# Performance work log

Hardware: AMD Instinct MI355X
Metric: run time of the kernel (lower is better)

## Reference

```python
import jax, jax.numpy as jnp
import numpy as np

N_NODES = 100000
N_EDGES = 1600000
N_FEATS = 128
HIDDEN = 20
N_GRAPHS = 256
N_CLASSES = 2


def setup_inputs() -> dict:
    key = jax.random.key(0)
    ks = jax.random.split(key, 12)
    x = jax.random.normal(ks[0], (N_NODES, N_FEATS), dtype=jnp.float32)
    edge_index = jax.random.randint(ks[1], (2, N_EDGES), 0, N_NODES, dtype=jnp.int64)
    batch = jnp.sort(jax.random.randint(ks[2], (N_NODES,), 0, N_GRAPHS, dtype=jnp.int64))
    def lin_init(k, fan_in, fan_out):
        kw, kb = jax.random.split(k)
        bound = 1.0 / np.sqrt(fan_in)
        W = jax.random.uniform(kw, (fan_in, fan_out), minval=-bound, maxval=bound, dtype=jnp.float32)
        b = jax.random.uniform(kb, (fan_out,), minval=-bound, maxval=bound, dtype=jnp.float32)
        return W, b
    W1, b1 = lin_init(ks[3], N_FEATS, HIDDEN)
    W2, b2 = lin_init(ks[4], HIDDEN, HIDDEN)
    W3, b3 = lin_init(ks[5], HIDDEN, HIDDEN)
    Wl, bl = lin_init(ks[6], 2 * HIDDEN, N_CLASSES)
    return {"x": x, "edge_index": edge_index, "batch": batch,
            "W1": W1, "b1": b1, "W2": W2, "b2": b2, "W3": W3, "b3": b3,
            "Wl": Wl, "bl": bl}


def gin_conv(x, src, dst, W, b):
    # GINConv with eps=0: mlp((1+eps)*x + sum_{j in N(i)} x_j)
    agg = jax.ops.segment_sum(x[src], dst, num_segments=x.shape[0])
    return (x + agg) @ W + b


def reference(x, edge_index, batch, W1, b1, W2, b2, W3, b3, Wl, bl):
    src, dst = edge_index[0], edge_index[1]
    h = jax.nn.relu(gin_conv(x, src, dst, W1, b1))
    h = jax.nn.relu(gin_conv(h, src, dst, W2, b2))
    h = jax.nn.relu(gin_conv(h, src, dst, W3, b3))  # [N, HIDDEN]
    # global max / mean pool per graph
    out1 = jax.ops.segment_max(h, batch, num_segments=N_GRAPHS)
    sums = jax.ops.segment_sum(h, batch, num_segments=N_GRAPHS)
    counts = jax.ops.segment_sum(jnp.ones((h.shape[0],), h.dtype), batch, num_segments=N_GRAPHS)
    out2 = sums / jnp.maximum(counts, 1.0)[:, None]
    pooled = jnp.concatenate([out1, out2], axis=-1)  # [G, 2*HIDDEN]
    return pooled @ Wl + bl
```

## Files before the change

kernel.cpp:

```cpp
#include <hip/hip_runtime.h>
#include <hip/hip_fp16.h>
#include <math.h>

#define N_NODES 100000
#define N_EDGES 1600000
#define N_FEATS 128
#define HIDDEN 20
#define N_GRAPHS 256

#define TILE 256
#define NB ((N_NODES + TILE - 1) / TILE)
#define SLOTS 5120
#define YSTRIDE 32

__device__ __half g_yh[2][(size_t)N_NODES * YSTRIDE];
__device__ float  g_facc[(size_t)N_NODES * HIDDEN];
__device__ int    g_part[(size_t)NB * SLOTS];
__device__ int    g_cursor[NB];
__device__ int    g_bbase[NB];
__device__ int    g_rowptr[N_NODES + 1];
__device__ int    g_col[N_EDGES];

__device__ __forceinline__ int detect_is64(const int* __restrict__ e32) {
    int acc = 0;
    #pragma unroll
    for (int j = 0; j < 8; j++) {
        int k = j * (N_EDGES / 8) + 997 * j + 13;
        acc |= e32[2 * k + 1];
    }
    return acc == 0;
}

__device__ __forceinline__ void load_edge(const void* eidx, int is64, int e,
                                          int& s, int& d) {
    if (is64) {
        const long long* e64 = (const long long*)eidx;
        s = (int)e64[e];
        d = (int)e64[N_EDGES + e];
    } else {
        const int* e32 = (const int*)eidx;
        s = e32[e];
        d = e32[N_EDGES + e];
    }
}

__global__ __launch_bounds__(512) void zero_kernel() {
    const int i = threadIdx.x;
    if (i < NB) g_cursor[i] = 0;
}

__global__ __launch_bounds__(512) void part_kernel(const void* __restrict__ eidx) {
    __shared__ int hist[NB];
    __shared__ int base[NB];
    const int t = threadIdx.x;
    const int e0 = blockIdx.x * 4096;
    for (int i = t; i < NB; i += 512) hist[i] = 0;
    const int is64 = detect_is64((const int*)eidx);
    __syncthreads();

    int sc[8], dc[8];
    #pragma unroll
    for (int k = 0; k < 8; k++) {
        const int e = e0 + k * 512 + t;
        sc[k] = -1; dc[k] = 0;
        if (e < N_EDGES) {
            int s, d;
            load_edge(eidx, is64, e, s, d);
            if ((unsigned)s < N_NODES && (unsigned)d < N_NODES) {
                sc[k] = s; dc[k] = d;
                atomicAdd(&hist[d >> 8], 1);
            }
        }
    }
    __syncthreads();
    for (int b = t; b < NB; b += 512) {
        const int c = hist[b];
        base[b] = c ? atomicAdd(&g_cursor[b], c) : 0;
        hist[b] = 0;
    }
    __syncthreads();
    #pragma unroll
    for (int k = 0; k < 8; k++) {
        if (sc[k] >= 0) {
            const int b = dc[k] >> 8;
            const int r = atomicAdd(&hist[b], 1);
            const int pos = base[b] + r;
            if (pos < SLOTS)
                g_part[(size_t)b * SLOTS + pos] = (sc[k] << 8) | (dc[k] & 255);
        }
    }
}

__global__ __launch_bounds__(512) void scanbase_kernel() {
    __shared__ int lds[512];
    const int t = threadIdx.x;
    int v = (t < NB) ? min(g_cursor[t], SLOTS) : 0;
    lds[t] = v;
    __syncthreads();
    for (int off = 1; off < 512; off <<= 1) {
        int u = (t >= off) ? lds[t - off] : 0;
        __syncthreads();
        lds[t] += u;
        __syncthreads();
    }
    if (t < NB) g_bbase[t] = lds[t] - v;
    if (t == 511) g_rowptr[N_NODES] = lds[511];
}

__global__ __launch_bounds__(512) void bucketsort_kernel() {
    __shared__ int hist[TILE];
    __shared__ int pfx[TILE];
    __shared__ int cur[TILE];
    __shared__ int sorted[SLOTS];
    const int t = threadIdx.x;
    const int b = blockIdx.x;
    const int cnt = min(g_cursor[b], SLOTS);
    const int base = g_bbase[b];
    if (t < TILE) hist[t] = 0;
    __syncthreads();
    const int* __restrict__ part = g_part + (size_t)b * SLOTS;
    for (int i = t; i < cnt; i += 512) atomicAdd(&hist[part[i] & 255], 1);
    __syncthreads();
    if (t < TILE) pfx[t] = hist[t];
    __syncthreads();
    for (int off = 1; off < TILE; off <<= 1) {
        int u = (t < TILE && t >= off) ? pfx[t - off] : 0;
        __syncthreads();
        if (t < TILE) pfx[t] += u;
        __syncthreads();
    }
    if (t < TILE) {
        const int ex = pfx[t] - hist[t];
        cur[t] = ex;
        const int node = b * TILE + t;
        if (node < N_NODES) g_rowptr[node] = base + ex;
    }
    __syncthreads();
    for (int i = t; i < cnt; i += 512) {
        const int rec = part[i];
        const int r = atomicAdd(&cur[rec & 255], 1);
        sorted[r] = rec >> 8;
    }
    __syncthreads();
    for (int i = t; i < cnt; i += 512) g_col[base + i] = sorted[i];
}

__global__ __launch_bounds__(256) void mm1_kernel(const float* __restrict__ x,
                                                  const float* __restrict__ W) {
    __shared__ float ldsWp[N_FEATS * HIDDEN];
    const int t = threadIdx.x;
    for (int i = t; i < N_FEATS * HIDDEN; i += 256) {
        const int korig = i / HIDDEN;
        const int c = i - korig * HIDDEN;
        const int jl = korig & 31;
        const int q = korig >> 5;
        ldsWp[(jl * 4 + q) * HIDDEN + c] = W[i];
    }
    __syncthreads();
    const int r = t >> 2;
    const int q = t & 3;
    const int row = blockIdx.x * 64 + r;
    const bool valid = row < N_NODES;

    float4 v[8];
    if (valid) {
        const float4* rp = (const float4*)&x[(size_t)row * N_FEATS + q * 32];
        #pragma unroll
        for (int i = 0; i < 8; i++) v[i] = rp[i];
    }
    float4 a0 = {0,0,0,0}, a1 = {0,0,0,0}, a2 = {0,0,0,0}, a3 = {0,0,0,0}, a4 = {0,0,0,0};
    if (valid) {
        #pragma unroll
        for (int i = 0; i < 8; i++) {
            const float xv[4] = {v[i].x, v[i].y, v[i].z, v[i].w};
            #pragma unroll
            for (int jj = 0; jj < 4; jj++) {
                const int jl = i * 4 + jj;
                const float4* wp = (const float4*)&ldsWp[(jl * 4 + q) * HIDDEN];
                const float xs = xv[jj];
                float4 w0 = wp[0], w1 = wp[1], w2 = wp[2], w3 = wp[3], w4 = wp[4];
                a0.x = fmaf(xs, w0.x, a0.x); a0.y = fmaf(xs, w0.y, a0.y);
                a0.z = fmaf(xs, w0.z, a0.z); a0.w = fmaf(xs, w0.w, a0.w);
                a1.x = fmaf(xs, w1.x, a1.x); a1.y = fmaf(xs, w1.y, a1.y);
                a1.z = fmaf(xs, w1.z, a1.z); a1.w = fmaf(xs, w1.w, a1.w);
                a2.x = fmaf(xs, w2.x, a2.x); a2.y = fmaf(xs, w2.y, a2.y);
                a2.z = fmaf(xs, w2.z, a2.z); a2.w = fmaf(xs, w2.w, a2.w);
                a3.x = fmaf(xs, w3.x, a3.x); a3.y = fmaf(xs, w3.y, a3.y);
                a3.z = fmaf(xs, w3.z, a3.z); a3.w = fmaf(xs, w3.w, a3.w);
                a4.x = fmaf(xs, w4.x, a4.x); a4.y = fmaf(xs, w4.y, a4.y);
                a4.z = fmaf(xs, w4.z, a4.z); a4.w = fmaf(xs, w4.w, a4.w);
            }
        }
    }
    float acc[20] = {a0.x, a0.y, a0.z, a0.w, a1.x, a1.y, a1.z, a1.w,
                     a2.x, a2.y, a2.z, a2.w, a3.x, a3.y, a3.z, a3.w,
                     a4.x, a4.y, a4.z, a4.w};
    #pragma unroll
    for (int off = 1; off <= 2; off <<= 1) {
        #pragma unroll
        for (int c = 0; c < 20; c++) acc[c] += __shfl_xor(acc[c], off);
    }
    if (valid) {
        __half* yp = &g_yh[0][(size_t)row * YSTRIDE];
        if (q == 0) {
            __half2 h0 = __float22half2_rn(make_float2(acc[0], acc[1]));
            __half2 h1 = __float22half2_rn(make_float2(acc[2], acc[3]));
            __half2 h2 = __float22half2_rn(make_float2(acc[4], acc[5]));
            __half2 h3 = __float22half2_rn(make_float2(acc[6], acc[7]));
            uint4 u; u.x = *(unsigned*)&h0; u.y = *(unsigned*)&h1;
            u.z = *(unsigned*)&h2; u.w = *(unsigned*)&h3;
            *(uint4*)&yp[0] = u;
        } else if (q == 1) {
            __half2 h0 = __float22half2_rn(make_float2(acc[8], acc[9]));
            __half2 h1 = __float22half2_rn(make_float2(acc[10], acc[11]));
            __half2 h2 = __float22half2_rn(make_float2(acc[12], acc[13]));
            __half2 h3 = __float22half2_rn(make_float2(acc[14], acc[15]));
            uint4 u; u.x = *(unsigned*)&h0; u.y = *(unsigned*)&h1;
            u.z = *(unsigned*)&h2; u.w = *(unsigned*)&h3;
            *(uint4*)&yp[8] = u;
        } else if (q == 2) {
            __half2 h0 = __float22half2_rn(make_float2(acc[16], acc[17]));
            __half2 h1 = __float22half2_rn(make_float2(acc[18], acc[19]));
            uint2 u; u.x = *(unsigned*)&h0; u.y = *(unsigned*)&h1;
            *(uint2*)&yp[16] = u;
        }
    }
}

template<bool FINAL>
__global__ __launch_bounds__(320) void gt_kernel(const float* __restrict__ bias,
                                                 const float* __restrict__ W,
                                                 int src) {
    const __half* __restrict__ y = g_yh[src];
    __shared__ float hrow[64][HIDDEN + 1];
    __shared__ float ldsW[HIDDEN * HIDDEN];
    __shared__ float ldsB[HIDDEN];
    const int t = threadIdx.x;
    if (!FINAL) {
        for (int i = t; i < HIDDEN * HIDDEN; i += 320) ldsW[i] = W[i];
        if (t < HIDDEN) ldsB[t] = bias[t];
    }
    const int nl = t / 5;
    const int chunk = t - nl * 5;
    const int node = blockIdx.x * 64 + nl;
    float sx = 0.f, sy = 0.f, sz = 0.f, sw = 0.f;
    if (node < N_NODES) {
        const int beg = g_rowptr[node];
        const int end = g_rowptr[node + 1];
        const int cb = chunk * 4;
        int i = beg;
        for (; i + 4 <= end; i += 4) {
            const int s0 = g_col[i + 0];
            const int s1 = g_col[i + 1];
            const int s2 = g_col[i + 2];
            const int s3 = g_col[i + 3];
            const uint2 u0 = *(const uint2*)&y[(size_t)s0 * YSTRIDE + cb];
            const uint2 u1 = *(const uint2*)&y[(size_t)s1 * YSTRIDE + cb];
            const uint2 u2 = *(const uint2*)&y[(size_t)s2 * YSTRIDE + cb];
            const uint2 u3 = *(const uint2*)&y[(size_t)s3 * YSTRIDE + cb];
            float2 a, b;
            a = __half22float2(*(const __half2*)&u0.x); b = __half22float2(*(const __half2*)&u0.y);
            sx += a.x; sy += a.y; sz += b.x; sw += b.y;
            a = __half22float2(*(const __half2*)&u1.x); b = __half22float2(*(const __half2*)&u1.y);
            sx += a.x; sy += a.y; sz += b.x; sw += b.y;
            a = __half22float2(*(const __half2*)&u2.x); b = __half22float2(*(const __half2*)&u2.y);
            sx += a.x; sy += a.y; sz += b.x; sw += b.y;
            a = __half22float2(*(const __half2*)&u3.x); b = __half22float2(*(const __half2*)&u3.y);
            sx += a.x; sy += a.y; sz += b.x; sw += b.y;
        }
        for (; i < end; i++) {
            const int s = g_col[i];
            const uint2 u = *(const uint2*)&y[(size_t)s * YSTRIDE + cb];
            const float2 f0 = __half22float2(*(const __half2*)&u.x);
            const float2 f1 = __half22float2(*(const __half2*)&u.y);
            sx += f0.x; sy += f0.y; sz += f1.x; sw += f1.y;
        }
        const uint2 u = *(const uint2*)&y[(size_t)node * YSTRIDE + cb];
        const float2 f0 = __half22float2(*(const __half2*)&u.x);
        const float2 f1 = __half22float2(*(const __half2*)&u.y);
        sx += f0.x; sy += f0.y; sz += f1.x; sw += f1.y;
    }
    if (FINAL) {
        if (node < N_NODES) {
            float4 o; o.x = sx; o.y = sy; o.z = sz; o.w = sw;
            *(float4*)&g_facc[(size_t)node * HIDDEN + chunk * 4] = o;
        }
        return;
    }
    if (node < N_NODES) {
        hrow[nl][chunk * 4 + 0] = sx;
        hrow[nl][chunk * 4 + 1] = sy;
        hrow[nl][chunk * 4 + 2] = sz;
        hrow[nl][chunk * 4 + 3] = sw;
    }
    __syncthreads();
    if (node < N_NODES) {
        float h[HIDDEN];
        #pragma unroll
        for (int c = 0; c < HIDDEN; c++) {
            float v = hrow[nl][c] + ldsB[c];
            h[c] = v > 0.f ? v : 0.f;
        }
        const int cb = chunk * 4;
        float s0 = 0.f, s1 = 0.f, s2 = 0.f, s3 = 0.f;
        #pragma unroll
        for (int k = 0; k < HIDDEN; k++) {
            const float* w = &ldsW[k * HIDDEN + cb];
            s0 = fmaf(h[k], w[0], s0);
            s1 = fmaf(h[k], w[1], s1);
            s2 = fmaf(h[k], w[2], s2);
            s3 = fmaf(h[k], w[3], s3);
        }
        __half2 o0 = __float22half2_rn(make_float2(s0, s1));
        __half2 o1 = __float22half2_rn(make_float2(s2, s3));
        uint2 u;
        u.x = *(unsigned*)&o0;
        u.y = *(unsigned*)&o1;
        *(uint2*)&g_yh[src ^ 1][(size_t)node * YSTRIDE + cb] = u;
    }
}

__global__ __launch_bounds__(256) void pool_kernel(const float* __restrict__ b3,
                                                   const void* __restrict__ batch,
                                                   const void* __restrict__ eidx,
                                                   const float* __restrict__ Wl,
                                                   const float* __restrict__ bl,
                                                   float* __restrict__ out) {
    const float* __restrict__ acc3 = g_facc;
    const int g = blockIdx.x;
    const int t = threadIdx.x;
    const int is64 = detect_is64((const int*)eidx);
    const int* b32 = (const int*)batch;
    const long long* b64 = (const long long*)batch;
    #define BAT(i) (is64 ? (int)b64[i] : b32[i])
    int lo = 0, hi = N_NODES;
    while (lo < hi) { int mid = (lo + hi) >> 1; if (BAT(mid) < g) lo = mid + 1; else hi = mid; }
    const int start = lo;
    lo = start; hi = N_NODES;
    while (lo < hi) { int mid = (lo + hi) >> 1; if (BAT(mid) < g + 1) lo = mid + 1; else hi = mid; }
    const int end = lo;
    #undef BAT

    float b3r[HIDDEN];
    #pragma unroll
    for (int c = 0; c < HIDDEN; c++) b3r[c] = b3[c];
    float mx[HIDDEN], sm[HIDDEN];
    #pragma unroll
    for (int c = 0; c < HIDDEN; c++) { mx[c] = 0.f; sm[c] = 0.f; }

    for (int i = start + t; i < end; i += 256) {
        const float4* rp = (const float4*)&acc3[(size_t)i * HIDDEN];
        float4 q[5] = {rp[0], rp[1], rp[2], rp[3], rp[4]};
        const float* r = (const float*)q;
        #pragma unroll
        for (int c = 0; c < HIDDEN; c++) {
            float v = r[c] + b3r[c];
            v = v > 0.f ? v : 0.f;
            mx[c] = fmaxf(mx[c], v);
            sm[c] += v;
        }
    }
    #pragma unroll
    for (int off = 32; off >= 1; off >>= 1) {
        #pragma unroll
        for (int c = 0; c < HIDDEN; c++) {
            mx[c] = fmaxf(mx[c], __shfl_xor(mx[c], off));
            sm[c] += __shfl_xor(sm[c], off);
        }
    }
    __shared__ float smx[4][HIDDEN];
    __shared__ float ssm[4][HIDDEN];
    const int wave = t >> 6, lane = t & 63;
    if (lane == 0) {
        #pragma unroll
        for (int c = 0; c < HIDDEN; c++) { smx[wave][c] = mx[c]; ssm[wave][c] = sm[c]; }
    }
    __syncthreads();
    if (t == 0) {
        float cnt = (float)(end - start);
        float pooled[2 * HIDDEN];
        #pragma unroll
        for (int c = 0; c < HIDDEN; c++) {
            float m = smx[0][c], s = ssm[0][c];
            #pragma unroll
            for (int w = 1; w < 4; w++) { m = fmaxf(m, smx[w][c]); s += ssm[w][c]; }
            pooled[c] = m;
            pooled[HIDDEN + c] = s / fmaxf(cnt, 1.f);
        }
        #pragma unroll
        for (int c = 0; c < 2; c++) {
            float o = bl[c];
            #pragma unroll
            for (int k = 0; k < 2 * HIDDEN; k++) o = fmaf(pooled[k], Wl[k * 2 + c], o);
            out[g * 2 + c] = o;
        }
    }
}

extern "C" void kernel_launch(void* const* d_in, const int* in_sizes, int n_in,
                              void* d_out, int out_size, void* d_ws, size_t ws_size,
                              hipStream_t stream) {
    const float* x    = (const float*)d_in[0];
    const void* eidx  = d_in[1];
    const void* batch = d_in[2];
    const float* W1  = (const float*)d_in[3];
    const float* b1  = (const float*)d_in[4];
    const float* W2  = (const float*)d_in[5];
    const float* b2  = (const float*)d_in[6];
    const float* W3  = (const float*)d_in[7];
    const float* b3  = (const float*)d_in[8];
    const float* Wl  = (const float*)d_in[9];
    const float* bl  = (const float*)d_in[10];
    float* out = (float*)d_out;
    (void)d_ws; (void)ws_size;

    const int mm1_blocks = (N_NODES + 63) / 64;
    const int gt_blocks  = (N_NODES + 63) / 64;

    zero_kernel<<<1, 512, 0, stream>>>();
    part_kernel<<<NB, 512, 0, stream>>>(eidx);
    scanbase_kernel<<<1, 512, 0, stream>>>();
    bucketsort_kernel<<<NB, 512, 0, stream>>>();

    mm1_kernel<<<mm1_blocks, 256, 0, stream>>>(x, W1);
    gt_kernel<false><<<gt_blocks, 320, 0, stream>>>(b1, W2, 0);
    gt_kernel<false><<<gt_blocks, 320, 0, stream>>>(b2, W3, 1);
    gt_kernel<true><<<gt_blocks, 320, 0, stream>>>(nullptr, nullptr, 0);
    pool_kernel<<<N_GRAPHS, 256, 0, stream>>>(b3, batch, eidx, Wl, bl, out);
}
```

Before: 173.8 us.

## Partition edges by source range to localize gathers, merge partial sums separately

Edges are now bucketed by destination tile and also by one of four source-node ranges. Each aggregation pass is split into a gather kernel that sums neighbours from a single source quarter, so the gathered feature rows occupy a smaller working set that fits better in cache, and writes fp16 partials per quarter. A second kernel adds the self term and the four partials, then applies bias, ReLU and the next linear layer. The cost is extra partial-buffer traffic, an additional fp16 rounding of the partial sums, twice as many launches, and a fixed slot cap of 1280 per bucket that could overflow on skewed graphs.

New measurement: 192.9 us. +11.0%, slower.

```diff
diff --git a/kernel.cpp b/kernel.cpp
--- a/kernel.cpp
+++ b/kernel.cpp
@@ -10,16 +10,20 @@
 
 #define TILE 256
 #define NB ((N_NODES + TILE - 1) / TILE)
-#define SLOTS 5120
+#define NQ 4
+#define QDIV 25000
+#define NB4 (NB * NQ)
+#define SLOTS4 1280
 #define YSTRIDE 32
 
 __device__ __half g_yh[2][(size_t)N_NODES * YSTRIDE];
+__device__ __half g_p16[NQ][(size_t)N_NODES * YSTRIDE];
 __device__ float  g_facc[(size_t)N_NODES * HIDDEN];
-__device__ int    g_part[(size_t)NB * SLOTS];
-__device__ int    g_cursor[NB];
-__device__ int    g_bbase[NB];
-__device__ int    g_rowptr[N_NODES + 1];
-__device__ int    g_col[N_EDGES];
+__device__ int    g_part[(size_t)NB4 * SLOTS4];
+__device__ int    g_cursor[NB4];
+__device__ int    g_rowbeg[NB4 * TILE];
+__device__ int    g_rowend[NB4 * TILE];
+__device__ int    g_col[(size_t)NB4 * SLOTS4];
 
 __device__ __forceinline__ int detect_is64(const int* __restrict__ e32) {
     int acc = 0;
@@ -45,16 +49,16 @@
 }
 
 __global__ __launch_bounds__(512) void zero_kernel() {
-    const int i = threadIdx.x;
-    if (i < NB) g_cursor[i] = 0;
+    const int i = blockIdx.x * 512 + threadIdx.x;
+    if (i < NB4) g_cursor[i] = 0;
 }
 
 __global__ __launch_bounds__(512) void part_kernel(const void* __restrict__ eidx) {
-    __shared__ int hist[NB];
-    __shared__ int base[NB];
+    __shared__ int hist[NB4];
+    __shared__ int base[NB4];
     const int t = threadIdx.x;
     const int e0 = blockIdx.x * 4096;
-    for (int i = t; i < NB; i += 512) hist[i] = 0;
+    for (int i = t; i < NB4; i += 512) hist[i] = 0;
     const int is64 = detect_is64((const int*)eidx);
     __syncthreads();
 
@@ -68,12 +72,12 @@
             load_edge(eidx, is64, e, s, d);
             if ((unsigned)s < N_NODES && (unsigned)d < N_NODES) {
                 sc[k] = s; dc[k] = d;
-                atomicAdd(&hist[d >> 8], 1);
+                atomicAdd(&hist[(d >> 8) * NQ + s / QDIV], 1);
             }
         }
     }
     __syncthreads();
-    for (int b = t; b < NB; b += 512) {
+    for (int b = t; b < NB4; b += 512) {
         const int c = hist[b];
         base[b] = c ? atomicAdd(&g_cursor[b], c) : 0;
         hist[b] = 0;
@@ -82,43 +86,27 @@
     #pragma unroll
     for (int k = 0; k < 8; k++) {
         if (sc[k] >= 0) {
-            const int b = dc[k] >> 8;
+            const int b = (dc[k] >> 8) * NQ + sc[k] / QDIV;
             const int r = atomicAdd(&hist[b], 1);
             const int pos = base[b] + r;
-            if (pos < SLOTS)
-                g_part[(size_t)b * SLOTS + pos] = (sc[k] << 8) | (dc[k] & 255);
-        }
-    }
-}
-
-__global__ __launch_bounds__(512) void scanbase_kernel() {
-    __shared__ int lds[512];
-    const int t = threadIdx.x;
-    int v = (t < NB) ? min(g_cursor[t], SLOTS) : 0;
-    lds[t] = v;
-    __syncthreads();
-    for (int off = 1; off < 512; off <<= 1) {
-        int u = (t >= off) ? lds[t - off] : 0;
-        __syncthreads();
-        lds[t] += u;
-        __syncthreads();
-    }
-    if (t < NB) g_bbase[t] = lds[t] - v;
-    if (t == 511) g_rowptr[N_NODES] = lds[511];
+            if (pos < SLOTS4)
+                g_part[(size_t)b * SLOTS4 + pos] = (sc[k] << 8) | (dc[k] & 255);
+        }
+    }
 }
 
 __global__ __launch_bounds__(512) void bucketsort_kernel() {
     __shared__ int hist[TILE];
     __shared__ int pfx[TILE];
     __shared__ int cur[TILE];
-    __shared__ int sorted[SLOTS];
+    __shared__ int sorted[SLOTS4];
     const int t = threadIdx.x;
     const int b = blockIdx.x;
-    const int cnt = min(g_cursor[b], SLOTS);
-    const int base = g_bbase[b];
+    const int cnt = min(g_cursor[b], SLOTS4);
+    const int base = b * SLOTS4;
     if (t < TILE) hist[t] = 0;
     __syncthreads();
-    const int* __restrict__ part = g_part + (size_t)b * SLOTS;
+    const int* __restrict__ part = g_part + (size_t)b * SLOTS4;
     for (int i = t; i < cnt; i += 512) atomicAdd(&hist[part[i] & 255], 1);
     __syncthreads();
     if (t < TILE) pfx[t] = hist[t];
@@ -132,8 +120,8 @@
     if (t < TILE) {
         const int ex = pfx[t] - hist[t];
         cur[t] = ex;
-        const int node = b * TILE + t;
-        if (node < N_NODES) g_rowptr[node] = base + ex;
+        g_rowbeg[b * TILE + t] = base + ex;
+        g_rowend[b * TILE + t] = base + ex + hist[t];
     }
     __syncthreads();
     for (int i = t; i < cnt; i += 512) {
@@ -227,27 +215,24 @@
     }
 }
 
-template<bool FINAL>
-__global__ __launch_bounds__(320) void gt_kernel(const float* __restrict__ bias,
-                                                 const float* __restrict__ W,
-                                                 int src) {
+__global__ __launch_bounds__(320) void gtA_kernel(int src) {
     const __half* __restrict__ y = g_yh[src];
-    __shared__ float hrow[64][HIDDEN + 1];
-    __shared__ float ldsW[HIDDEN * HIDDEN];
-    __shared__ float ldsB[HIDDEN];
-    const int t = threadIdx.x;
-    if (!FINAL) {
-        for (int i = t; i < HIDDEN * HIDDEN; i += 320) ldsW[i] = W[i];
-        if (t < HIDDEN) ldsB[t] = bias[t];
-    }
-    const int nl = t / 5;
-    const int chunk = t - nl * 5;
-    const int node = blockIdx.x * 64 + nl;
-    float sx = 0.f, sy = 0.f, sz = 0.f, sw = 0.f;
-    if (node < N_NODES) {
-        const int beg = g_rowptr[node];
-        const int end = g_rowptr[node + 1];
-        const int cb = chunk * 4;
+    const int b = blockIdx.x;
+    const int tile = b >> 2;
+    const int j = b & 3;
+    const int t = threadIdx.x;
+    const int nlb = t / 5;
+    const int chunk = t - nlb * 5;
+    const int cb = chunk * 4;
+    #pragma unroll
+    for (int it = 0; it < 4; it++) {
+        const int dl = it * 64 + nlb;
+        const int node = tile * TILE + dl;
+        if (node >= N_NODES) break;
+        const int idx = b * TILE + dl;
+        const int beg = g_rowbeg[idx];
+        const int end = g_rowend[idx];
+        float sx = 0.f, sy = 0.f, sz = 0.f, sw = 0.f;
         int i = beg;
         for (; i + 4 <= end; i += 4) {
             const int s0 = g_col[i + 0];
@@ -258,15 +243,15 @@
             const uint2 u1 = *(const uint2*)&y[(size_t)s1 * YSTRIDE + cb];
             const uint2 u2 = *(const uint2*)&y[(size_t)s2 * YSTRIDE + cb];
             const uint2 u3 = *(const uint2*)&y[(size_t)s3 * YSTRIDE + cb];
-            float2 a, b;
-            a = __half22float2(*(const __half2*)&u0.x); b = __half22float2(*(const __half2*)&u0.y);
-            sx += a.x; sy += a.y; sz += b.x; sw += b.y;
-            a = __half22float2(*(const __half2*)&u1.x); b = __half22float2(*(const __half2*)&u1.y);
-            sx += a.x; sy += a.y; sz += b.x; sw += b.y;
-            a = __half22float2(*(const __half2*)&u2.x); b = __half22float2(*(const __half2*)&u2.y);
-            sx += a.x; sy += a.y; sz += b.x; sw += b.y;
-            a = __half22float2(*(const __half2*)&u3.x); b = __half22float2(*(const __half2*)&u3.y);
-            sx += a.x; sy += a.y; sz += b.x; sw += b.y;
+            float2 a, c;
+            a = __half22float2(*(const __half2*)&u0.x); c = __half22float2(*(const __half2*)&u0.y);
+            sx += a.x; sy += a.y; sz += c.x; sw += c.y;
+            a = __half22float2(*(const __half2*)&u1.x); c = __half22float2(*(const __half2*)&u1.y);
+            sx += a.x; sy += a.y; sz += c.x; sw += c.y;
+            a = __half22float2(*(const __half2*)&u2.x); c = __half22float2(*(const __half2*)&u2.y);
+            sx += a.x; sy += a.y; sz += c.x; sw += c.y;
+            a = __half22float2(*(const __half2*)&u3.x); c = __half22float2(*(const __half2*)&u3.y);
+            sx += a.x; sy += a.y; sz += c.x; sw += c.y;
         }
         for (; i < end; i++) {
             const int s = g_col[i];
@@ -275,23 +260,57 @@
             const float2 f1 = __half22float2(*(const __half2*)&u.y);
             sx += f0.x; sy += f0.y; sz += f1.x; sw += f1.y;
         }
-        const uint2 u = *(const uint2*)&y[(size_t)node * YSTRIDE + cb];
-        const float2 f0 = __half22float2(*(const __half2*)&u.x);
-        const float2 f1 = __half22float2(*(const __half2*)&u.y);
-        sx += f0.x; sy += f0.y; sz += f1.x; sw += f1.y;
+        __half2 o0 = __float22half2_rn(make_float2(sx, sy));
+        __half2 o1 = __float22half2_rn(make_float2(sz, sw));
+        uint2 u; u.x = *(unsigned*)&o0; u.y = *(unsigned*)&o1;
+        *(uint2*)&g_p16[j][(size_t)node * YSTRIDE + cb] = u;
+    }
+}
+
+template<bool FINAL>
+__global__ __launch_bounds__(320) void gtB_kernel(const float* __restrict__ bias,
+                                                  const float* __restrict__ W,
+                                                  int src) {
+    const __half* __restrict__ y = g_yh[src];
+    __shared__ float hrow[64][HIDDEN + 1];
+    __shared__ float ldsW[HIDDEN * HIDDEN];
+    __shared__ float ldsB[HIDDEN];
+    const int t = threadIdx.x;
+    if (!FINAL) {
+        for (int i = t; i < HIDDEN * HIDDEN; i += 320) ldsW[i] = W[i];
+        if (t < HIDDEN) ldsB[t] = bias[t];
+    }
+    const int nl = t / 5;
+    const int chunk = t - nl * 5;
+    const int cb = chunk * 4;
+    const int node = blockIdx.x * 64 + nl;
+    float sx = 0.f, sy = 0.f, sz = 0.f, sw = 0.f;
+    if (node < N_NODES) {
+        const size_t off = (size_t)node * YSTRIDE + cb;
+        uint2 u = *(const uint2*)&y[off];
+        float2 f0 = __half22float2(*(const __half2*)&u.x);
+        float2 f1 = __half22float2(*(const __half2*)&u.y);
+        sx = f0.x; sy = f0.y; sz = f1.x; sw = f1.y;
+        #pragma unroll
+        for (int j = 0; j < NQ; j++) {
+            const uint2 p = *(const uint2*)&g_p16[j][off];
+            f0 = __half22float2(*(const __half2*)&p.x);
+            f1 = __half22float2(*(const __half2*)&p.y);
+            sx += f0.x; sy += f0.y; sz += f1.x; sw += f1.y;
+        }
     }
     if (FINAL) {
         if (node < N_NODES) {
             float4 o; o.x = sx; o.y = sy; o.z = sz; o.w = sw;
-            *(float4*)&g_facc[(size_t)node * HIDDEN + chunk * 4] = o;
+            *(float4*)&g_facc[(size_t)node * HIDDEN + cb] = o;
         }
         return;
     }
     if (node < N_NODES) {
-        hrow[nl][chunk * 4 + 0] = sx;
-        hrow[nl][chunk * 4 + 1] = sy;
-        hrow[nl][chunk * 4 + 2] = sz;
-        hrow[nl][chunk * 4 + 3] = sw;
+        hrow[nl][cb + 0] = sx;
+        hrow[nl][cb + 1] = sy;
+        hrow[nl][cb + 2] = sz;
+        hrow[nl][cb + 3] = sw;
     }
     __syncthreads();
     if (node < N_NODES) {
@@ -301,7 +320,6 @@
             float v = hrow[nl][c] + ldsB[c];
             h[c] = v > 0.f ? v : 0.f;
         }
-        const int cb = chunk * 4;
         float s0 = 0.f, s1 = 0.f, s2 = 0.f, s3 = 0.f;
         #pragma unroll
         for (int k = 0; k < HIDDEN; k++) {
@@ -415,16 +433,18 @@
     (void)d_ws; (void)ws_size;
 
     const int mm1_blocks = (N_NODES + 63) / 64;
-    const int gt_blocks  = (N_NODES + 63) / 64;
-
-    zero_kernel<<<1, 512, 0, stream>>>();
+    const int gtB_blocks = (N_NODES + 63) / 64;
+
+    zero_kernel<<<4, 512, 0, stream>>>();
     part_kernel<<<NB, 512, 0, stream>>>(eidx);
-    scanbase_kernel<<<1, 512, 0, stream>>>();
-    bucketsort_kernel<<<NB, 512, 0, stream>>>();
+    bucketsort_kernel<<<NB4, 512, 0, stream>>>();
 
     mm1_kernel<<<mm1_blocks, 256, 0, stream>>>(x, W1);
-    gt_kernel<false><<<gt_blocks, 320, 0, stream>>>(b1, W2, 0);
-    gt_kernel<false><<<gt_blocks, 320, 0, stream>>>(b2, W3, 1);
-    gt_kernel<true><<<gt_blocks, 320, 0, stream>>>(nullptr, nullptr, 0);
+    gtA_kernel<<<NB4, 320, 0, stream>>>(0);
+    gtB_kernel<false><<<gtB_blocks, 320, 0, stream>>>(b1, W2, 0);
+    gtA_kernel<<<NB4, 320, 0, stream>>>(1);
+    gtB_kernel<false><<<gtB_blocks, 320, 0, stream>>>(b2, W3, 1);
+    gtA_kernel<<<NB4, 320, 0, stream>>>(0);
+    gtB_kernel<true><<<gtB_blocks, 320, 0, stream>>>(nullptr, nullptr, 0);
     pool_kernel<<<N_GRAPHS, 256, 0, stream>>>(b3, batch, eidx, Wl, bl, out);
 }
```
